# Performance work log

Measured on AMD Instinct MI355X. Metric: run time of the kernel, lower is better.

Reference implementation:

```python
import math
import jax, jax.numpy as jnp
import numpy as np

DIM = 256
HEADS = 4
TAU = 1e-3
TOPK = 64


def setup_inputs() -> dict:
    key = jax.random.key(0)
    ks = jax.random.split(key, 11)
    B, N, D = 4, 1024, DIM
    s = 1.0 / math.sqrt(D)
    return {
        "F_cls": jax.random.normal(ks[0], (B, N, D), jnp.float32),
        "F_seg": jax.random.normal(ks[1], (B, N, D), jnp.float32),
        "F_age": jax.random.normal(ks[2], (B, N, D), jnp.float32),
        "Wq": jax.random.normal(ks[3], (D, D), jnp.float32) * s,
        "bq": jnp.zeros((D,), jnp.float32),
        "Wk": jax.random.normal(ks[4], (D, D), jnp.float32) * s,
        "bk": jnp.zeros((D,), jnp.float32),
        "Wv": jax.random.normal(ks[5], (D, D), jnp.float32) * s,
        "bv": jnp.zeros((D,), jnp.float32),
        "Wo": jax.random.normal(ks[6], (D, D), jnp.float32) * s,
        "bo": jnp.zeros((D,), jnp.float32),
    }


def reference(F_cls, F_seg, F_age, Wq, bq, Wk, bk, Wv, bv, Wo, bo):
    # Concatenate the three task branches along tokens: (B, 3N, D)
    X = jnp.concatenate([F_cls, F_seg, F_age], axis=1)
    # L1 soft-thresholding
    Xs = jnp.sign(X) * jnp.maximum(jnp.abs(X) - TAU, 0.0)
    B, TN, D = Xs.shape
    N = F_cls.shape[1]
    H, Dh = HEADS, D // HEADS
    # per-sample channel saliency and top-k channel mask
    sal = jnp.abs(Xs).mean(axis=1)                      # (B, D)
    _, idx = jax.lax.top_k(sal, TOPK)                   # (B, k)
    mask = jnp.zeros((B, D), bool).at[jnp.arange(B)[:, None], idx].set(True)
    Xt = Xs * mask[:, None, :]                          # (B, TN, D)
    # shared K/V over all tokens; Q over all tokens equals the concat of the
    # three per-branch q_proj outputs (same weights), so one fused attention
    # is mathematically identical to the three original calls.
    Q = Xt @ Wq.T + bq
    K = Xt @ Wk.T + bk
    V = Xt @ Wv.T + bv
    def heads(x):
        return x.reshape(B, TN, H, Dh).transpose(0, 2, 1, 3)  # (B,H,TN,Dh)
    Qh, Kh, Vh = heads(Q), heads(K), heads(V)
    logits = jnp.einsum("bhqd,bhkd->bhqk", Qh, Kh) / math.sqrt(Dh)
    A = jax.nn.softmax(logits, axis=-1)
    out = jnp.einsum("bhqk,bhkd->bhqd", A, Vh)
    out = out.transpose(0, 2, 1, 3).reshape(B, TN, D)
    out = out @ Wo.T + bo
    return (out[:, 0:N], out[:, N:2 * N], out[:, 2 * N:3 * N])
```

## Files before the change

kernel.cpp:

```cpp
#include <hip/hip_runtime.h>
#include <math.h>

typedef __attribute__((ext_vector_type(8))) short bf16x8;
typedef __attribute__((ext_vector_type(16))) float f32x16;

#define Bsz 4
#define Nn 1024
#define TN 3072
#define Dd 256
#define Hh 4
#define DH 64
#define TAUc 1e-3f
#define QSCALE 0.1803368801111f

#define SALP_OFF 0
#define IDX_OFF  98304
#define XCB_OFF  98560
#define WCT_OFF  491776
#define QB_OFF   590080
#define KB_OFF   2162944
#define VT_OFF   3735808
#define OP0_OFF  5308672
#define OP1_OFF  8454400
#define SML_OFF  11600128

__device__ __forceinline__ ushort f2b(float f) {
    uint u = __float_as_uint(f);
    u += 0x7fffu + ((u >> 16) & 1u);
    return (ushort)(u >> 16);
}
__device__ __forceinline__ uint pk2(float a, float b) {
    return (uint)f2b(a) | ((uint)f2b(b) << 16);
}
__device__ __forceinline__ uint trunc_pk(float a, float b) {
    return (__float_as_uint(a) >> 16) | (__float_as_uint(b) & 0xFFFF0000u);
}
__device__ __forceinline__ float hi_f(float a) {
    return __uint_as_float(__float_as_uint(a) & 0xFFFF0000u);
}
__device__ __forceinline__ uint cvtpk(float a, float b) {
    uint r;
    asm("v_cvt_pk_bf16_f32 %0, %1, %2" : "=v"(r) : "v"(a), "v"(b));
    return r;
}
union U4B8 { uint u[4]; bf16x8 v; };
__device__ __forceinline__ bf16x8 ld8(const ushort* p) { return *(const bf16x8*)p; }

__global__ __launch_bounds__(256) void k_sal(
        const float* __restrict__ F0, const float* __restrict__ F1,
        const float* __restrict__ F2, float* __restrict__ salp) {
    int b = blockIdx.x / 96;
    int slab = blockIdx.x - b * 96;
    int t0 = slab * 32;
    int seg = t0 >> 10, tt0 = t0 & 1023;
    const float* F = (seg == 0) ? F0 : (seg == 1 ? F1 : F2);
    const float* base = &F[(size_t)((b << 10) + tt0) * Dd + threadIdx.x];
    float acc = 0.f;
    #pragma unroll 4
    for (int r = 0; r < 32; ++r) {
        float x = base[(size_t)r * Dd];
        acc += fmaxf(fabsf(x) - TAUc, 0.f);
    }
    salp[blockIdx.x * 256 + threadIdx.x] = acc;
}

__global__ void k_topk(const float* __restrict__ salp, int* __restrict__ idx) {
    __shared__ float v[256];
    __shared__ int cnt;
    int b = blockIdx.x, tid = threadIdx.x;
    float myval = 0.f;
    const float* p = &salp[(size_t)b * 96 * 256 + tid];
    #pragma unroll 4
    for (int s = 0; s < 96; ++s) myval += p[s * 256];
    v[tid] = myval;
    if (tid == 0) cnt = 0;
    __syncthreads();
    for (int k = 2; k <= 256; k <<= 1)
        for (int j = k >> 1; j > 0; j >>= 1) {
            int ixj = tid ^ j;
            if (ixj > tid) {
                float a = v[tid], c = v[ixj];
                bool up = ((tid & k) == 0);
                if ((a > c) == up) { v[tid] = c; v[ixj] = a; }
            }
            __syncthreads();
        }
    float thr = v[192];
    if (myval >= thr) {
        int p2 = atomicAdd(&cnt, 1);
        if (p2 < 64) idx[b * 64 + p2] = tid;
    }
}

__global__ __launch_bounds__(256) void k_gather(
        const float* __restrict__ F0, const float* __restrict__ F1,
        const float* __restrict__ F2,
        const float* __restrict__ Wq, const float* __restrict__ Wk,
        const float* __restrict__ Wv, const int* __restrict__ idx,
        uint* __restrict__ Xcb, uint* __restrict__ Wct) {
    __shared__ float xs[32 * 260];
    __shared__ int ids[64];
    int tid = threadIdx.x;
    if (blockIdx.x < 384) {
        int b = blockIdx.x / 96;
        int t0 = (blockIdx.x - b * 96) * 32;
        if (tid < 64) ids[tid] = idx[b * 64 + tid];
        int seg = t0 >> 10, tt0 = t0 & 1023;
        const float* F = (seg == 0) ? F0 : (seg == 1 ? F1 : F2);
        const float* base = &F[(size_t)((b << 10) + tt0) * Dd];
        #pragma unroll
        for (int i = 0; i < 8; ++i) {
            int i0 = tid + i * 256;
            int r = i0 >> 6, c4 = (i0 & 63) << 2;
            float4 x = *(const float4*)&base[(size_t)r * Dd + c4];
            x.x = copysignf(fmaxf(fabsf(x.x) - TAUc, 0.f), x.x);
            x.y = copysignf(fmaxf(fabsf(x.y) - TAUc, 0.f), x.y);
            x.z = copysignf(fmaxf(fabsf(x.z) - TAUc, 0.f), x.z);
            x.w = copysignf(fmaxf(fabsf(x.w) - TAUc, 0.f), x.w);
            *(float4*)&xs[r * 260 + c4] = x;
        }
        __syncthreads();
        #pragma unroll
        for (int i = 0; i < 4; ++i) {
            int i0 = tid + i * 256;
            int r = i0 >> 5, jp = i0 & 31;
            float x0 = xs[r * 260 + ids[2 * jp]];
            float x1 = xs[r * 260 + ids[2 * jp + 1]];
            Xcb[(size_t)(b * TN + t0 + r) * 32 + jp] = pk2(x0, x1);
        }
    } else {
        int gid = (blockIdx.x - 384) * 256 + tid;
        int b = gid / 24576;
        if (tid < 64) ids[tid] = idx[b * 64 + tid];
        __syncthreads();
        int rem = gid - b * 24576;
        int mat = rem / 8192;
        int rem2 = rem - mat * 8192;
        int dout = rem2 >> 5, jp = rem2 & 31;
        const float* Wm = (mat == 0) ? Wq : (mat == 1 ? Wk : Wv);
        float w0 = Wm[(size_t)dout * 256 + ids[2 * jp]];
        float w1 = Wm[(size_t)dout * 256 + ids[2 * jp + 1]];
        Wct[((size_t)(b * 3 + mat) * 256 + dout) * 32 + jp] = pk2(w0, w1);
    }
}

__global__ __launch_bounds__(256) void k_qkv(
        const ushort* __restrict__ Xcb, const ushort* __restrict__ Wct,
        const float* __restrict__ bq, const float* __restrict__ bk,
        const float* __restrict__ bv,
        ushort* __restrict__ Qh, ushort* __restrict__ Kh, ushort* __restrict__ Vt) {
    int wave = threadIdx.x >> 6, lane = threadIdx.x & 63;
    int l31 = lane & 31, h = lane >> 5;
    int W = blockIdx.x * 4 + wave;
    int b = W / 576;
    int r = W - b * 576;
    int mat = r / 192;
    int p = r - mat * 192;
    const ushort* Xb = Xcb + (size_t)b * TN * 64;
    const ushort* Wm = Wct + (size_t)(b * 3 + mat) * 256 * 64;
    f32x16 c[4];
    #pragma unroll
    for (int nt = 0; nt < 4; ++nt)
        #pragma unroll
        for (int q = 0; q < 16; ++q) c[nt][q] = 0.f;
    if (mat < 2) {
        int mtt = p % 96, ng = p / 96;
        const ushort* arow = &Xb[(size_t)(mtt * 32 + l31) * 64];
        #pragma unroll
        for (int kc = 0; kc < 4; ++kc) {
            bf16x8 af = ld8(arow + kc * 16 + 8 * h);
            #pragma unroll
            for (int nt = 0; nt < 4; ++nt) {
                bf16x8 bf = ld8(&Wm[(size_t)(ng * 128 + nt * 32 + l31) * 64 + kc * 16 + 8 * h]);
                c[nt] = __builtin_amdgcn_mfma_f32_32x32x16_bf16(af, bf, c[nt], 0, 0, 0);
            }
        }
        const float* bias = mat ? bk : bq;
        float sc = mat ? 1.0f : QSCALE;
        ushort* Out = mat ? Kh : Qh;
        #pragma unroll
        for (int nt = 0; nt < 4; ++nt) {
            int dout = ng * 128 + nt * 32 + l31;
            int head = dout >> 6, d63 = dout & 63;
            float bb = bias[dout];
            size_t obase = ((size_t)(b * 4 + head) * TN + mtt * 32) * 64 + d63;
            #pragma unroll
            for (int u = 0; u < 16; ++u) {
                int trow = (u & 3) + 8 * (u >> 2) + 4 * h;
                Out[obase + (size_t)trow * 64] = f2b((c[nt][u] + bb) * sc);
            }
        }
    } else {
        int mtv = p & 7, tg = p >> 3;
        const ushort* arow = &Wm[(size_t)(mtv * 32 + l31) * 64];
        #pragma unroll
        for (int kc = 0; kc < 4; ++kc) {
            bf16x8 af = ld8(arow + kc * 16 + 8 * h);
            #pragma unroll
            for (int nt = 0; nt < 4; ++nt) {
                bf16x8 bf = ld8(&Xb[(size_t)(tg * 128 + nt * 32 + l31) * 64 + kc * 16 + 8 * h]);
                c[nt] = __builtin_amdgcn_mfma_f32_32x32x16_bf16(af, bf, c[nt], 0, 0, 0);
            }
        }
        int head = mtv >> 1;
        int sl = (l31 & 19) | ((l31 & 4) << 1) | ((l31 & 8) >> 1);
        #pragma unroll
        for (int nt = 0; nt < 4; ++nt) {
            size_t tslot = (size_t)(tg * 128 + nt * 32 + sl);
            #pragma unroll
            for (int u = 0; u < 16; ++u) {
                int dout = mtv * 32 + (u & 3) + 8 * (u >> 2) + 4 * h;
                int d63 = dout & 63;
                Vt[((size_t)(b * 4 + head) * 64 + d63) * TN + tslot] =
                    f2b(c[nt][u] + bv[dout]);
            }
        }
    }
}

__global__ __launch_bounds__(256, 3) void k_attn(
        const ushort* __restrict__ Qg, const ushort* __restrict__ Kg,
        const ushort* __restrict__ Vtg,
        float* __restrict__ OP0, float* __restrict__ OP1,
        float* __restrict__ Sml) {
    __shared__ __align__(16) ushort Ks[128 * 64];
    __shared__ __align__(16) ushort Vts[64 * 128];
    int bh = blockIdx.x / 48;
    int rem = blockIdx.x - bh * 48;
    int qt = rem >> 1, ks = rem & 1;
    int b = bh >> 2, hh = bh & 3;
    int tid = threadIdx.x, wave = tid >> 6, lane = tid & 63;
    int l31 = lane & 31, h = lane >> 5;
    const ushort* Kb = Kg + (size_t)bh * TN * DH;
    const ushort* Vtb = Vtg + (size_t)bh * DH * TN;
    int q0 = qt * 128 + wave * 32;
    const ushort* Qb = Qg + ((size_t)bh * TN + q0 + l31) * DH;
    bf16x8 qf[4];
    #pragma unroll
    for (int kc = 0; kc < 4; ++kc) qf[kc] = ld8(&Qb[kc * 16 + 8 * h]);

    int krow0 = tid >> 3, kcc = tid & 7;
    int vrow0 = tid >> 4, vch = tid & 15;
    int kt0 = ks * 1536;
    const ushort* KbL = Kb + (size_t)(kt0 + krow0) * 64 + kcc * 8;
    const ushort* VtL = Vtb + (size_t)vrow0 * TN + kt0 + vch * 8;

    f32x16 o0, o1;
    #pragma unroll
    for (int q = 0; q < 16; ++q) { o0[q] = 0.f; o1[q] = 0.f; }
    float lrun = 0.f;

    int fq0 = (l31 ^ (l31 >> 3)) & 7;
    int fq1 = ((32 + l31) ^ ((32 + l31) >> 3)) & 7;

    #pragma unroll 1
    for (int it = 0; it < 12; ++it) {
        __syncthreads();
        #pragma unroll
        for (int i = 0; i < 4; ++i) {
            int kr = krow0 + 32 * i;
            int fk = (kr ^ (kr >> 3)) & 7;
            *(uint4*)&Ks[kr * 64 + ((kcc ^ fk) << 3)] =
                *(const uint4*)(KbL + (size_t)(32 * i) * 64);
            int vr = vrow0 + 16 * i;
            int fv = (vr ^ (vr >> 3)) & 7;
            *(uint4*)&Vts[vr * 128 + (((vch & 8) | ((vch & 7) ^ fv)) << 3)] =
                *(const uint4*)(VtL + (size_t)(16 * i) * TN);
        }
        KbL += 128 * 64;
        VtL += 128;
        __syncthreads();

        uint pkA[32];
        float psum = 0.f;
        #pragma unroll
        for (int hf = 0; hf < 2; ++hf) {
            f32x16 s0, s1;
            #pragma unroll
            for (int q = 0; q < 16; ++q) { s0[q] = 0.f; s1[q] = 0.f; }
            int r0 = hf * 64 + l31, r1 = r0 + 32;
            #pragma unroll
            for (int kc = 0; kc < 4; ++kc) {
                int ch = 2 * kc + h;
                bf16x8 k0 = ld8(&Ks[r0 * 64 + ((ch ^ fq0) << 3)]);
                bf16x8 k1 = ld8(&Ks[r1 * 64 + ((ch ^ fq1) << 3)]);
                s0 = __builtin_amdgcn_mfma_f32_32x32x16_bf16(k0, qf[kc], s0, 0, 0, 0);
                s1 = __builtin_amdgcn_mfma_f32_32x32x16_bf16(k1, qf[kc], s1, 0, 0, 0);
            }
            #pragma unroll
            for (int u = 0; u < 8; ++u) {
                float pa = exp2f(s0[2 * u]), pb = exp2f(s0[2 * u + 1]);
                psum += pa + pb;
                pkA[hf * 16 + u] = cvtpk(pa, pb);
            }
            #pragma unroll
            for (int u = 0; u < 8; ++u) {
                float pa = exp2f(s1[2 * u]), pb = exp2f(s1[2 * u + 1]);
                psum += pa + pb;
                pkA[hf * 16 + 8 + u] = cvtpk(pa, pb);
            }
        }
        psum += __shfl_xor(psum, 32);
        lrun += psum;

        #pragma unroll
        for (int kc2 = 0; kc2 < 8; ++kc2) {
            U4B8 pf;
            pf.u[0] = pkA[4 * kc2];     pf.u[1] = pkA[4 * kc2 + 1];
            pf.u[2] = pkA[4 * kc2 + 2]; pf.u[3] = pkA[4 * kc2 + 3];
            int ch = 2 * kc2 + h;
            bf16x8 v0f = ld8(&Vts[l31 * 128 + (((ch & 8) | ((ch & 7) ^ fq0)) << 3)]);
            bf16x8 v1f = ld8(&Vts[(32 + l31) * 128 + (((ch & 8) | ((ch & 7) ^ fq1)) << 3)]);
            o0 = __builtin_amdgcn_mfma_f32_32x32x16_bf16(pf.v, v0f, o0, 0, 0, 0);
            o1 = __builtin_amdgcn_mfma_f32_32x32x16_bf16(pf.v, v1f, o1, 0, 0, 0);
        }
    }

    float* OP = ks ? OP1 : OP0;
    #pragma unroll
    for (int q = 0; q < 16; ++q) {
        int qrow = (q & 3) + 8 * (q >> 2) + 4 * h;
        int t = q0 + qrow;
        size_t base = ((size_t)b * TN + t) * Dd + hh * 64;
        OP[base + l31] = o0[q];
        OP[base + 32 + l31] = o1[q];
    }
    if (h == 0)
        Sml[(size_t)ks * 49152 + (size_t)bh * TN + q0 + l31] = lrun;
}

__global__ __launch_bounds__(256) void k_out(
        const float* __restrict__ OP0, const float* __restrict__ OP1,
        const float* __restrict__ Sml, const float* __restrict__ Wo,
        const float* __restrict__ bo, float* __restrict__ out) {
    __shared__ __align__(16) ushort Mhi[64 * 16];
    __shared__ __align__(16) ushort Mlo[64 * 16];
    __shared__ float invsh[64 * 4];
    int nd4 = blockIdx.x;
    int R0 = blockIdx.y * 64;
    int b = R0 / TN;
    int tloc0 = R0 - b * TN;
    int tid = threadIdx.x, wave = tid >> 6, lane = tid & 63;
    int l31 = lane & 31, h = lane >> 5;
    int wt = wave & 1, wd = wave >> 1;
    {
        int hd = tid >> 6, t = tid & 63;
        size_t o = (size_t)(b * 4 + hd) * TN + tloc0 + t;
        invsh[t * 4 + hd] = 1.f / (Sml[o] + Sml[49152 + o]);
    }
    int dout = nd4 * 64 + wd * 32 + l31;
    float bb = bo[dout];
    const float* wrow = &Wo[(size_t)dout * 256];
    int st_t = tid >> 2, st_c = tid & 3;
    size_t st_base = ((size_t)(b * TN + tloc0 + st_t)) * 256 + st_c * 4;
    f32x16 acc;
    #pragma unroll
    for (int q = 0; q < 16; ++q) acc[q] = 0.f;
    #pragma unroll 1
    for (int st = 0; st < 16; ++st) {
        __syncthreads();
        int hd = st >> 2;
        {
            size_t ob = st_base + st * 16;
            float4 x = *(const float4*)&OP0[ob];
            float4 y = *(const float4*)&OP1[ob];
            float s = invsh[st_t * 4 + hd];
            float m0 = (x.x + y.x) * s, m1 = (x.y + y.y) * s;
            float m2 = (x.z + y.z) * s, m3 = (x.w + y.w) * s;
            uint2 wh = { trunc_pk(m0, m1), trunc_pk(m2, m3) };
            uint2 wl = { trunc_pk(m0 - hi_f(m0), m1 - hi_f(m1)),
                         trunc_pk(m2 - hi_f(m2), m3 - hi_f(m3)) };
            *(uint2*)&Mhi[st_t * 16 + st_c * 4] = wh;
            *(uint2*)&Mlo[st_t * 16 + st_c * 4] = wl;
        }
        __syncthreads();
        int din0 = st * 16 + 8 * h;
        float4 w0 = *(const float4*)&wrow[din0];
        float4 w1 = *(const float4*)&wrow[din0 + 4];
        U4B8 wh, wl;
        wh.u[0] = trunc_pk(w0.x, w0.y); wh.u[1] = trunc_pk(w0.z, w0.w);
        wh.u[2] = trunc_pk(w1.x, w1.y); wh.u[3] = trunc_pk(w1.z, w1.w);
        wl.u[0] = trunc_pk(w0.x - hi_f(w0.x), w0.y - hi_f(w0.y));
        wl.u[1] = trunc_pk(w0.z - hi_f(w0.z), w0.w - hi_f(w0.w));
        wl.u[2] = trunc_pk(w1.x - hi_f(w1.x), w1.y - hi_f(w1.y));
        wl.u[3] = trunc_pk(w1.z - hi_f(w1.z), w1.w - hi_f(w1.w));
        int trow = wt * 32 + l31;
        bf16x8 ah = *(const bf16x8*)&Mhi[trow * 16 + 8 * h];
        bf16x8 al = *(const bf16x8*)&Mlo[trow * 16 + 8 * h];
        acc = __builtin_amdgcn_mfma_f32_32x32x16_bf16(ah, wh.v, acc, 0, 0, 0);
        acc = __builtin_amdgcn_mfma_f32_32x32x16_bf16(al, wh.v, acc, 0, 0, 0);
        acc = __builtin_amdgcn_mfma_f32_32x32x16_bf16(ah, wl.v, acc, 0, 0, 0);
    }
    #pragma unroll
    for (int u = 0; u < 16; ++u) {
        int tloc = tloc0 + wt * 32 + (u & 3) + 8 * (u >> 2) + 4 * h;
        int chunk = tloc >> 10, tt = tloc & 1023;
        out[(size_t)chunk * (Bsz * Nn * Dd) + ((size_t)(b * Nn + tt)) * Dd + dout] =
            acc[u] + bb;
    }
}

extern "C" void kernel_launch(void* const* d_in, const int* in_sizes, int n_in,
                              void* d_out, int out_size, void* d_ws, size_t ws_size,
                              hipStream_t stream) {
    const float* F0 = (const float*)d_in[0];
    const float* F1 = (const float*)d_in[1];
    const float* F2 = (const float*)d_in[2];
    const float* Wq = (const float*)d_in[3];
    const float* bq = (const float*)d_in[4];
    const float* Wk = (const float*)d_in[5];
    const float* bk = (const float*)d_in[6];
    const float* Wv = (const float*)d_in[7];
    const float* bv = (const float*)d_in[8];
    const float* Wo = (const float*)d_in[9];
    const float* bo = (const float*)d_in[10];
    float* ws = (float*)d_ws;
    float* out = (float*)d_out;

    int* idxp = (int*)(ws + IDX_OFF);
    uint* Xcb = (uint*)(ws + XCB_OFF);
    uint* Wct = (uint*)(ws + WCT_OFF);
    ushort* Qb16 = (ushort*)(ws + QB_OFF);
    ushort* Kb16 = (ushort*)(ws + KB_OFF);
    ushort* Vt16 = (ushort*)(ws + VT_OFF);
    float* OP0 = ws + OP0_OFF;
    float* OP1 = ws + OP1_OFF;
    float* Sml = ws + SML_OFF;

    k_sal<<<384, 256, 0, stream>>>(F0, F1, F2, ws + SALP_OFF);
    k_topk<<<Bsz, 256, 0, stream>>>(ws + SALP_OFF, idxp);
    k_gather<<<768, 256, 0, stream>>>(F0, F1, F2, Wq, Wk, Wv, idxp, Xcb, Wct);
    k_qkv<<<576, 256, 0, stream>>>((const ushort*)Xcb, (const ushort*)Wct,
                                   bq, bk, bv, Qb16, Kb16, Vt16);
    k_attn<<<768, 256, 0, stream>>>(Qb16, Kb16, Vt16, OP0, OP1, Sml);
    k_out<<<dim3(4, 192), 256, 0, stream>>>(OP0, OP1, Sml, Wo, bo, out);
}
```

Before: 194.2 us.

## Pre-swizzle K/V tiles in projection and stream via global_load_lds; double-buffer out-proj

The projection kernel now writes K and V^T directly in the tiled, XOR-swizzled layout that the attention kernel keeps in LDS. The attention kernel can then copy each tile with contiguous global_load_lds DMA instead of computing per-thread swizzled register round-trips. The output-projection kernel moves to 32-wide K stages with a double-buffered, swizzled LDS tile, which halves the barrier count and overlaps the next stage's load with the current MFMAs. The cost is scattered 2-byte stores in the projection epilogue and coupling of the layouts across kernels.

```diff
diff --git a/kernel.cpp b/kernel.cpp
--- a/kernel.cpp
+++ b/kernel.cpp
@@ -42,6 +42,11 @@
     uint r;
     asm("v_cvt_pk_bf16_f32 %0, %1, %2" : "=v"(r) : "v"(a), "v"(b));
     return r;
+}
+__device__ __forceinline__ void gld16(const ushort* g, ushort* l) {
+    __builtin_amdgcn_global_load_lds(
+        (const __attribute__((address_space(1))) uint*)g,
+        (__attribute__((address_space(3))) uint*)l, 16, 0, 0);
 }
 union U4B8 { uint u[4]; bf16x8 v; };
 __device__ __forceinline__ bf16x8 ld8(const ushort* p) { return *(const bf16x8*)p; }
@@ -175,19 +180,35 @@
                 c[nt] = __builtin_amdgcn_mfma_f32_32x32x16_bf16(af, bf, c[nt], 0, 0, 0);
             }
         }
-        const float* bias = mat ? bk : bq;
-        float sc = mat ? 1.0f : QSCALE;
-        ushort* Out = mat ? Kh : Qh;
-        #pragma unroll
-        for (int nt = 0; nt < 4; ++nt) {
-            int dout = ng * 128 + nt * 32 + l31;
-            int head = dout >> 6, d63 = dout & 63;
-            float bb = bias[dout];
-            size_t obase = ((size_t)(b * 4 + head) * TN + mtt * 32) * 64 + d63;
-            #pragma unroll
-            for (int u = 0; u < 16; ++u) {
-                int trow = (u & 3) + 8 * (u >> 2) + 4 * h;
-                Out[obase + (size_t)trow * 64] = f2b((c[nt][u] + bb) * sc);
+        if (mat == 0) {
+            #pragma unroll
+            for (int nt = 0; nt < 4; ++nt) {
+                int dout = ng * 128 + nt * 32 + l31;
+                int head = dout >> 6, d63 = dout & 63;
+                float bb = bq[dout];
+                size_t obase = ((size_t)(b * 4 + head) * TN + mtt * 32) * 64 + d63;
+                #pragma unroll
+                for (int u = 0; u < 16; ++u) {
+                    int trow = (u & 3) + 8 * (u >> 2) + 4 * h;
+                    Qh[obase + (size_t)trow * 64] = f2b((c[nt][u] + bb) * QSCALE);
+                }
+            }
+        } else {
+            #pragma unroll
+            for (int nt = 0; nt < 4; ++nt) {
+                int dout = ng * 128 + nt * 32 + l31;
+                int head = dout >> 6, d63 = dout & 63;
+                float bb = bk[dout];
+                size_t base = (size_t)(b * 4 + head) * 196608;
+                #pragma unroll
+                for (int u = 0; u < 16; ++u) {
+                    int trow = (u & 3) + 8 * (u >> 2) + 4 * h;
+                    int t = mtt * 32 + trow;
+                    int row = t & 127, tile = t >> 7;
+                    int fk = (row ^ (row >> 3)) & 7;
+                    Kh[base + (size_t)tile * 8192 + row * 64 +
+                       (((d63 >> 3) ^ fk) << 3) + (d63 & 7)] = f2b(c[nt][u] + bb);
+                }
             }
         }
     } else {
@@ -204,15 +225,18 @@
         }
         int head = mtv >> 1;
         int sl = (l31 & 19) | ((l31 & 4) << 1) | ((l31 & 8) >> 1);
+        size_t vbase = (size_t)(b * 4 + head) * 196608 + (size_t)tg * 8192;
         #pragma unroll
         for (int nt = 0; nt < 4; ++nt) {
-            size_t tslot = (size_t)(tg * 128 + nt * 32 + sl);
+            int cc = (nt * 32 + sl) >> 3;
+            int elem = sl & 7;
             #pragma unroll
             for (int u = 0; u < 16; ++u) {
                 int dout = mtv * 32 + (u & 3) + 8 * (u >> 2) + 4 * h;
-                int d63 = dout & 63;
-                Vt[((size_t)(b * 4 + head) * 64 + d63) * TN + tslot] =
-                    f2b(c[nt][u] + bv[dout]);
+                int row = dout & 63;
+                int fv = (row ^ (row >> 3)) & 7;
+                int ch = (cc & 8) | ((cc & 7) ^ fv);
+                Vt[vbase + row * 128 + ch * 8 + elem] = f2b(c[nt][u] + bv[dout]);
             }
         }
     }
@@ -231,19 +255,14 @@
     int b = bh >> 2, hh = bh & 3;
     int tid = threadIdx.x, wave = tid >> 6, lane = tid & 63;
     int l31 = lane & 31, h = lane >> 5;
-    const ushort* Kb = Kg + (size_t)bh * TN * DH;
-    const ushort* Vtb = Vtg + (size_t)bh * DH * TN;
     int q0 = qt * 128 + wave * 32;
     const ushort* Qb = Qg + ((size_t)bh * TN + q0 + l31) * DH;
     bf16x8 qf[4];
     #pragma unroll
     for (int kc = 0; kc < 4; ++kc) qf[kc] = ld8(&Qb[kc * 16 + 8 * h]);
 
-    int krow0 = tid >> 3, kcc = tid & 7;
-    int vrow0 = tid >> 4, vch = tid & 15;
-    int kt0 = ks * 1536;
-    const ushort* KbL = Kb + (size_t)(kt0 + krow0) * 64 + kcc * 8;
-    const ushort* VtL = Vtb + (size_t)vrow0 * TN + kt0 + vch * 8;
+    const ushort* Kt = Kg + (size_t)bh * 196608 + (size_t)(ks * 12) * 8192 + tid * 8;
+    const ushort* Vtt = Vtg + (size_t)bh * 196608 + (size_t)(ks * 12) * 8192 + tid * 8;
 
     f32x16 o0, o1;
     #pragma unroll
@@ -258,17 +277,10 @@
         __syncthreads();
         #pragma unroll
         for (int i = 0; i < 4; ++i) {
-            int kr = krow0 + 32 * i;
-            int fk = (kr ^ (kr >> 3)) & 7;
-            *(uint4*)&Ks[kr * 64 + ((kcc ^ fk) << 3)] =
-                *(const uint4*)(KbL + (size_t)(32 * i) * 64);
-            int vr = vrow0 + 16 * i;
-            int fv = (vr ^ (vr >> 3)) & 7;
-            *(uint4*)&Vts[vr * 128 + (((vch & 8) | ((vch & 7) ^ fv)) << 3)] =
-                *(const uint4*)(VtL + (size_t)(16 * i) * TN);
-        }
-        KbL += 128 * 64;
-        VtL += 128;
+            gld16(Kt + i * 2048, &Ks[(tid + i * 256) * 8]);
+            gld16(Vtt + i * 2048, &Vts[(tid + i * 256) * 8]);
+        }
+        Kt += 8192; Vtt += 8192;
         __syncthreads();
 
         uint pkA[32];
@@ -333,8 +345,7 @@
         const float* __restrict__ OP0, const float* __restrict__ OP1,
         const float* __restrict__ Sml, const float* __restrict__ Wo,
         const float* __restrict__ bo, float* __restrict__ out) {
-    __shared__ __align__(16) ushort Mhi[64 * 16];
-    __shared__ __align__(16) ushort Mlo[64 * 16];
+    __shared__ __align__(16) ushort Ms[2][64][64];
     __shared__ float invsh[64 * 4];
     int nd4 = blockIdx.x;
     int R0 = blockIdx.y * 64;
@@ -352,44 +363,60 @@
     float bb = bo[dout];
     const float* wrow = &Wo[(size_t)dout * 256];
     int st_t = tid >> 2, st_c = tid & 3;
-    size_t st_base = ((size_t)(b * TN + tloc0 + st_t)) * 256 + st_c * 4;
+    int fst = (st_t ^ (st_t >> 3)) & 7;
+    size_t gbase = ((size_t)(b * TN + tloc0 + st_t)) * 256 + st_c * 8;
+    int trow = wt * 32 + l31;
+    int ftr = (trow ^ (trow >> 3)) & 7;
     f32x16 acc;
     #pragma unroll
     for (int q = 0; q < 16; ++q) acc[q] = 0.f;
+
+    auto stage_load = [&](int st, int buf) {
+        size_t ob = gbase + (size_t)st * 32;
+        float4 x0 = *(const float4*)&OP0[ob];
+        float4 x1 = *(const float4*)&OP0[ob + 4];
+        float4 y0 = *(const float4*)&OP1[ob];
+        float4 y1 = *(const float4*)&OP1[ob + 4];
+        float s = invsh[st_t * 4 + (st >> 1)];
+        float m0 = (x0.x + y0.x) * s, m1 = (x0.y + y0.y) * s;
+        float m2 = (x0.z + y0.z) * s, m3 = (x0.w + y0.w) * s;
+        float m4 = (x1.x + y1.x) * s, m5 = (x1.y + y1.y) * s;
+        float m6 = (x1.z + y1.z) * s, m7 = (x1.w + y1.w) * s;
+        uint4 hi = { trunc_pk(m0, m1), trunc_pk(m2, m3),
+                     trunc_pk(m4, m5), trunc_pk(m6, m7) };
+        uint4 lo = { trunc_pk(m0 - hi_f(m0), m1 - hi_f(m1)),
+                     trunc_pk(m2 - hi_f(m2), m3 - hi_f(m3)),
+                     trunc_pk(m4 - hi_f(m4), m5 - hi_f(m5)),
+                     trunc_pk(m6 - hi_f(m6), m7 - hi_f(m7)) };
+        *(uint4*)&Ms[buf][st_t][(st_c ^ fst) * 8] = hi;
+        *(uint4*)&Ms[buf][st_t][((4 + st_c) ^ fst) * 8] = lo;
+    };
+
+    __syncthreads();
+    stage_load(0, 0);
     #pragma unroll 1
-    for (int st = 0; st < 16; ++st) {
+    for (int st = 0; st < 8; ++st) {
         __syncthreads();
-        int hd = st >> 2;
-        {
-            size_t ob = st_base + st * 16;
-            float4 x = *(const float4*)&OP0[ob];
-            float4 y = *(const float4*)&OP1[ob];
-            float s = invsh[st_t * 4 + hd];
-            float m0 = (x.x + y.x) * s, m1 = (x.y + y.y) * s;
-            float m2 = (x.z + y.z) * s, m3 = (x.w + y.w) * s;
-            uint2 wh = { trunc_pk(m0, m1), trunc_pk(m2, m3) };
-            uint2 wl = { trunc_pk(m0 - hi_f(m0), m1 - hi_f(m1)),
-                         trunc_pk(m2 - hi_f(m2), m3 - hi_f(m3)) };
-            *(uint2*)&Mhi[st_t * 16 + st_c * 4] = wh;
-            *(uint2*)&Mlo[st_t * 16 + st_c * 4] = wl;
-        }
-        __syncthreads();
-        int din0 = st * 16 + 8 * h;
-        float4 w0 = *(const float4*)&wrow[din0];
-        float4 w1 = *(const float4*)&wrow[din0 + 4];
-        U4B8 wh, wl;
-        wh.u[0] = trunc_pk(w0.x, w0.y); wh.u[1] = trunc_pk(w0.z, w0.w);
-        wh.u[2] = trunc_pk(w1.x, w1.y); wh.u[3] = trunc_pk(w1.z, w1.w);
-        wl.u[0] = trunc_pk(w0.x - hi_f(w0.x), w0.y - hi_f(w0.y));
-        wl.u[1] = trunc_pk(w0.z - hi_f(w0.z), w0.w - hi_f(w0.w));
-        wl.u[2] = trunc_pk(w1.x - hi_f(w1.x), w1.y - hi_f(w1.y));
-        wl.u[3] = trunc_pk(w1.z - hi_f(w1.z), w1.w - hi_f(w1.w));
-        int trow = wt * 32 + l31;
-        bf16x8 ah = *(const bf16x8*)&Mhi[trow * 16 + 8 * h];
-        bf16x8 al = *(const bf16x8*)&Mlo[trow * 16 + 8 * h];
-        acc = __builtin_amdgcn_mfma_f32_32x32x16_bf16(ah, wh.v, acc, 0, 0, 0);
-        acc = __builtin_amdgcn_mfma_f32_32x32x16_bf16(al, wh.v, acc, 0, 0, 0);
-        acc = __builtin_amdgcn_mfma_f32_32x32x16_bf16(ah, wl.v, acc, 0, 0, 0);
+        if (st < 7) stage_load(st + 1, (st + 1) & 1);
+        int buf = st & 1;
+        #pragma unroll
+        for (int kc = 0; kc < 2; ++kc) {
+            bf16x8 ah = *(const bf16x8*)&Ms[buf][trow][((2 * kc + h) ^ ftr) * 8];
+            bf16x8 al = *(const bf16x8*)&Ms[buf][trow][((4 + 2 * kc + h) ^ ftr) * 8];
+            int din0 = st * 32 + kc * 16 + 8 * h;
+            float4 w0 = *(const float4*)&wrow[din0];
+            float4 w1 = *(const float4*)&wrow[din0 + 4];
+            U4B8 wh, wl;
+            wh.u[0] = trunc_pk(w0.x, w0.y); wh.u[1] = trunc_pk(w0.z, w0.w);
+            wh.u[2] = trunc_pk(w1.x, w1.y); wh.u[3] = trunc_pk(w1.z, w1.w);
+            wl.u[0] = trunc_pk(w0.x - hi_f(w0.x), w0.y - hi_f(w0.y));
+            wl.u[1] = trunc_pk(w0.z - hi_f(w0.z), w0.w - hi_f(w0.w));
+            wl.u[2] = trunc_pk(w1.x - hi_f(w1.x), w1.y - hi_f(w1.y));
+            wl.u[3] = trunc_pk(w1.z - hi_f(w1.z), w1.w - hi_f(w1.w));
+            acc = __builtin_amdgcn_mfma_f32_32x32x16_bf16(ah, wh.v, acc, 0, 0, 0);
+            acc = __builtin_amdgcn_mfma_f32_32x32x16_bf16(al, wh.v, acc, 0, 0, 0);
+            acc = __builtin_amdgcn_mfma_f32_32x32x16_bf16(ah, wl.v, acc, 0, 0, 0);
+        }
     }
     #pragma unroll
     for (int u = 0; u < 16; ++u) {
```

Measured after the change: 187.8 us. 3.3% less time.
